# Optimization experiments

Measured on AMD Instinct MI355X. Metric: run time of the kernel, lower is better.

## Reference

```python
import jax, jax.numpy as jnp
import numpy as np

DIM = 512
HEADS = 8
HD = DIM // HEADS
WS = 4          # window_size
SHIFT = 2       # window_size // 2
HID = 4 * DIM   # mlp hidden
EPS = 1e-5


def _ln(x, g, b):
    m = jnp.mean(x, axis=-1, keepdims=True)
    v = jnp.mean((x - m) ** 2, axis=-1, keepdims=True)
    return (x - m) * jax.lax.rsqrt(v + EPS) * g + b


def setup_inputs() -> dict:
    key = jax.random.key(0)
    ks = jax.random.split(key, 12)
    s = 0.02
    return {
        "x": jax.random.normal(ks[0], (2, 32, 32, 32, DIM), dtype=jnp.float32),
        "ln1_g": jnp.ones((DIM,), jnp.float32),
        "ln1_b": jnp.zeros((DIM,), jnp.float32),
        "qkv_w": jax.random.normal(ks[1], (DIM, 3 * DIM), jnp.float32) * s,
        "qkv_b": jnp.zeros((3 * DIM,), jnp.float32),
        "proj_w": jax.random.normal(ks[2], (DIM, DIM), jnp.float32) * s,
        "proj_b": jnp.zeros((DIM,), jnp.float32),
        "ln2_g": jnp.ones((DIM,), jnp.float32),
        "ln2_b": jnp.zeros((DIM,), jnp.float32),
        "ffn_w1": jax.random.normal(ks[3], (DIM, HID), jnp.float32) * s,
        "ffn_b1": jnp.zeros((HID,), jnp.float32),
        "ffn_w2": jax.random.normal(ks[4], (HID, DIM), jnp.float32) * s,
        "ffn_b2": jnp.zeros((DIM,), jnp.float32),
    }


def reference(x, ln1_g, ln1_b, qkv_w, qkv_b, proj_w, proj_b,
              ln2_g, ln2_b, ffn_w1, ffn_b1, ffn_w2, ffn_b2):
    B, D, H, W, C = x.shape
    nD, nH, nW = D // WS, H // WS, W // WS
    N = WS ** 3

    # cyclic shift
    xs = jnp.roll(x, (-SHIFT, -SHIFT, -SHIFT), axis=(1, 2, 3))

    # window partition: (B*numWin, N, C)
    xw = xs.reshape(B, nD, WS, nH, WS, nW, WS, C)
    xw = xw.transpose(0, 1, 3, 5, 2, 4, 6, 7).reshape(-1, N, C)

    # pre-norm attention
    h = _ln(xw, ln1_g, ln1_b)
    qkv = (h @ qkv_w + qkv_b).reshape(-1, N, 3, HEADS, HD)
    q, k, v = jnp.moveaxis(qkv, 2, 0)          # each (Bn, N, HEADS, HD)
    scale = HD ** -0.5
    logits = jnp.einsum('bnhd,bmhd->bhnm', q, k) * scale
    attn = jax.nn.softmax(logits, axis=-1)
    out = jnp.einsum('bhnm,bmhd->bnhd', attn, v).reshape(-1, N, C)
    out = out @ proj_w + proj_b
    xw = xw + out

    # window reverse + unshift
    xo = xw.reshape(B, nD, nH, nW, WS, WS, WS, C)
    xo = xo.transpose(0, 1, 4, 2, 5, 3, 6, 7).reshape(B, D, H, W, C)
    xo = jnp.roll(xo, (SHIFT, SHIFT, SHIFT), axis=(1, 2, 3))

    # pre-norm FFN (exact GELU, dropout inactive in eval)
    h2 = _ln(xo, ln2_g, ln2_b)
    ffn = jax.nn.gelu(h2 @ ffn_w1 + ffn_b1, approximate=False) @ ffn_w2 + ffn_b2
    return xo + ffn
```

## Files before the change

### kernel.cpp

```cpp
#include <hip/hip_runtime.h>
#include <hip/hip_bf16.h>


typedef __attribute__((ext_vector_type(4))) short short4v;
typedef __attribute__((ext_vector_type(8))) short short8v;
typedef __attribute__((ext_vector_type(4))) float f32x4;

__device__ __forceinline__ unsigned short f2bf(float f) {
  unsigned u = __float_as_uint(f);
  u += 0x7fffu + ((u >> 16) & 1u);
  return (unsigned short)(u >> 16);
}

__device__ __forceinline__ void gload_lds16(const unsigned short* g, unsigned short* l) {
  __builtin_amdgcn_global_load_lds(
      (const __attribute__((address_space(1))) unsigned int*)g,
      (__attribute__((address_space(3))) unsigned int*)l, 16, 0, 0);
}

__global__ __launch_bounds__(256)
void wprep_all(const float* __restrict__ qkv_w, const float* __restrict__ proj_w,
               const float* __restrict__ w1, const float* __restrict__ w2,
               unsigned short* __restrict__ wt) {
  int idx = blockIdx.x * 256 + threadIdx.x;
  const float* w; int kbits, N, base;
  if (idx < 786432)       { w = qkv_w;  kbits = 9;  N = 1536; base = 0; }
  else if (idx < 1048576) { w = proj_w; kbits = 9;  N = 512;  base = 786432; }
  else if (idx < 2097152) { w = w1;     kbits = 9;  N = 2048; base = 1048576; }
  else                    { w = w2;     kbits = 11; N = 512;  base = 2097152; }
  int li = idx - base;
  int K = 1 << kbits;
  int n = li >> kbits, kk = li & (K - 1);
  wt[idx] = f2bf(w[(long)kk * N + n]);
}

__global__ __launch_bounds__(256)
void ln_kernel(const float* __restrict__ src, const float* __restrict__ g,
               const float* __restrict__ bb, unsigned short* __restrict__ dst,
               const int gather) {
  const int lane = threadIdx.x & 63;
  const int row = blockIdx.x * 4 + (threadIdx.x >> 6);
  long srow;
  if (gather) {
    int n = row & 63, win = row >> 6;
    int w0 = win & 7, h0 = (win >> 3) & 7, d0 = (win >> 6) & 7, b2 = win >> 9;
    int dx = n & 3, dy = (n >> 2) & 3, dz = n >> 4;
    int od = (d0 * 4 + dz + 2) & 31, oh = (h0 * 4 + dy + 2) & 31, ow = (w0 * 4 + dx + 2) & 31;
    srow = (((long)b2 * 32 + od) * 32 + oh) * 32 + ow;
  } else {
    srow = row;
  }
  const float4* sp = (const float4*)(src + srow * 512);
  float4 x0 = sp[lane], x1 = sp[lane + 64];
  float sum = x0.x + x0.y + x0.z + x0.w + x1.x + x1.y + x1.z + x1.w;
  float sq  = x0.x*x0.x + x0.y*x0.y + x0.z*x0.z + x0.w*x0.w
            + x1.x*x1.x + x1.y*x1.y + x1.z*x1.z + x1.w*x1.w;
#pragma unroll
  for (int off = 1; off < 64; off <<= 1) {
    sum += __shfl_xor(sum, off, 64);
    sq  += __shfl_xor(sq, off, 64);
  }
  float mean = sum * (1.0f / 512.0f);
  float var  = sq * (1.0f / 512.0f) - mean * mean;
  float rstd = rsqrtf(var + 1e-5f);
  float4 g0 = ((const float4*)g)[lane], g1 = ((const float4*)g)[lane + 64];
  float4 b0 = ((const float4*)bb)[lane], b1v = ((const float4*)bb)[lane + 64];
  ushort4 o0, o1;
  o0.x = f2bf((x0.x - mean) * rstd * g0.x + b0.x);
  o0.y = f2bf((x0.y - mean) * rstd * g0.y + b0.y);
  o0.z = f2bf((x0.z - mean) * rstd * g0.z + b0.z);
  o0.w = f2bf((x0.w - mean) * rstd * g0.w + b0.w);
  o1.x = f2bf((x1.x - mean) * rstd * g1.x + b1v.x);
  o1.y = f2bf((x1.y - mean) * rstd * g1.y + b1v.y);
  o1.z = f2bf((x1.z - mean) * rstd * g1.z + b1v.z);
  o1.w = f2bf((x1.w - mean) * rstd * g1.w + b1v.w);
  *(ushort4*)(dst + (long)row * 512 + lane * 4) = o0;
  *(ushort4*)(dst + (long)row * 512 + 256 + lane * 4) = o1;
}

template <int EPI>
__global__ __launch_bounds__(512, 2)
void gemm_bt(const unsigned short* __restrict__ A,
             const unsigned short* __restrict__ Bt,
             const float* __restrict__ bias, int K,
             void* __restrict__ out0,
             unsigned short* __restrict__ out1,
             unsigned short* __restrict__ out2,
             const float* __restrict__ res) {
  __shared__ unsigned short As[2][256 * 64];
  __shared__ unsigned short Bs[2][256 * 64];
  const int tid = threadIdx.x;
  const int lane = tid & 63;
  const int wv = tid >> 6;
  const int wm = wv >> 2;
  const int wn = wv & 3;
  const int quad = lane >> 4;
  const int l15 = lane & 15;

  const int gx = gridDim.x;
  const int nwg = gx * gridDim.y;
  const int bid = blockIdx.y * gx + blockIdx.x;
  const int cpx = nwg >> 3;
  const int wg2 = (bid & 7) * cpx + (bid >> 3);
  const int bx = wg2 % gx;
  const int by = wg2 / gx;
  const long row0 = (long)by * 256;
  const long col0 = (long)bx * 256;

  f32x4 acc[8][4] = {};

  const int srow = wv * 8 + (lane >> 3);
  const int scg  = (lane & 7) ^ (lane >> 3);
  const unsigned short* gA = A  + (row0 + srow) * K + scg * 8;
  const unsigned short* gB = Bt + (col0 + srow) * K + scg * 8;
  const long jmp = 64L * K;
  const int ldst = wv * 512;

#define STAGE_A(buf, koff) do {                                         \
    _Pragma("unroll")                                                   \
    for (int j = 0; j < 4; ++j)                                         \
      gload_lds16(gA + (koff) + j * jmp, &As[buf][ldst + j * 4096]);    \
  } while (0)
#define STAGE_B(buf, koff) do {                                         \
    _Pragma("unroll")                                                   \
    for (int j = 0; j < 4; ++j)                                         \
      gload_lds16(gB + (koff) + j * jmp, &Bs[buf][ldst + j * 4096]);    \
  } while (0)

  const int co0 = ((quad)     ^ (l15 & 7)) * 8;
  const int co1 = ((quad + 4) ^ (l15 & 7)) * 8;
  const int aB0 = (wm * 128 + l15) * 64 + co0;
  const int aB1 = (wm * 128 + l15) * 64 + co1;
  const int bB0 = (wn * 64 + l15) * 64 + co0;
  const int bB1 = (wn * 64 + l15) * 64 + co1;

#define MFMA_ROW(mh)                                                    \
    _Pragma("unroll")                                                   \
    for (int i = 0; i < 4; ++i)                                         \
      _Pragma("unroll")                                                 \
      for (int nt = 0; nt < 4; ++nt)                                    \
        acc[(mh) * 4 + i][nt] = __builtin_amdgcn_mfma_f32_16x16x32_bf16( \
            af[i], bfrag[nt], acc[(mh) * 4 + i][nt], 0, 0, 0)

  const int nk = K >> 6;
  STAGE_A(0, 0);
  STAGE_B(0, 0);
  asm volatile("s_waitcnt vmcnt(0)" ::: "memory");
  __builtin_amdgcn_s_barrier();

  for (int t = 0; t < nk; ++t) {
    const int cur = t & 1, nxt = cur ^ 1;
    const int more = (t + 1 < nk);
    const int kn = (t + 1) << 6;
    const unsigned short* Ac = As[cur];
    const unsigned short* Bc = Bs[cur];
    short8v bfrag[4];
    {
      short8v af[4];
#pragma unroll
      for (int nt = 0; nt < 4; ++nt) bfrag[nt] = *(const short8v*)&Bc[bB0 + nt * 1024];
#pragma unroll
      for (int i = 0; i < 4; ++i) af[i] = *(const short8v*)&Ac[aB0 + i * 1024];
      if (more) STAGE_A(nxt, kn);
      __builtin_amdgcn_s_barrier();
      __builtin_amdgcn_s_setprio(1);
      MFMA_ROW(0);
      __builtin_amdgcn_s_setprio(0);
      __builtin_amdgcn_s_barrier();
    }
    {
      short8v af[4];
#pragma unroll
      for (int i = 0; i < 4; ++i) af[i] = *(const short8v*)&Ac[aB0 + (4 + i) * 1024];
      if (more) STAGE_B(nxt, kn);
      __builtin_amdgcn_s_barrier();
      __builtin_amdgcn_s_setprio(1);
      MFMA_ROW(1);
      __builtin_amdgcn_s_setprio(0);
      __builtin_amdgcn_s_barrier();
    }
    {
      short8v af[4];
#pragma unroll
      for (int nt = 0; nt < 4; ++nt) bfrag[nt] = *(const short8v*)&Bc[bB1 + nt * 1024];
#pragma unroll
      for (int i = 0; i < 4; ++i) af[i] = *(const short8v*)&Ac[aB1 + i * 1024];
      __builtin_amdgcn_s_barrier();
      __builtin_amdgcn_s_setprio(1);
      MFMA_ROW(0);
      __builtin_amdgcn_s_setprio(0);
      __builtin_amdgcn_s_barrier();
    }
    {
      short8v af[4];
#pragma unroll
      for (int i = 0; i < 4; ++i) af[i] = *(const short8v*)&Ac[aB1 + (4 + i) * 1024];
      __builtin_amdgcn_s_barrier();
      __builtin_amdgcn_s_setprio(1);
      MFMA_ROW(1);
      __builtin_amdgcn_s_setprio(0);
      asm volatile("s_waitcnt vmcnt(0)" ::: "memory");
      __builtin_amdgcn_s_barrier();
    }
  }
#undef STAGE_A
#undef STAGE_B
#undef MFMA_ROW

#pragma unroll
  for (int mt = 0; mt < 8; ++mt) {
#pragma unroll
    for (int nt = 0; nt < 4; ++nt) {
#pragma unroll
      for (int r = 0; r < 4; ++r) {
        const long gr = row0 + wm * 128 + mt * 16 + quad * 4 + r;
        const long gc = col0 + wn * 64 + nt * 16 + l15;
        float val = acc[mt][nt][r] + bias[gc];
        if (EPI == 0) {
          int which = (int)(gc >> 9), rem = (int)gc & 511;
          int head = rem >> 6, hd = rem & 63;
          long win = gr >> 6, n = gr & 63;
          long base = (win * 8 + head) * 4096;
          unsigned short bv = f2bf(val);
          if (which == 0)      ((unsigned short*)out0)[base + n * 64 + hd] = bv;
          else if (which == 1) out1[base + n * 64 + hd] = bv;
          else                 out2[base + hd * 64 + n] = bv;
        } else if (EPI == 1) {
          int win = (int)(gr >> 6), n = (int)gr & 63;
          int w0 = win & 7, h0 = (win >> 3) & 7, d0 = (win >> 6) & 7, b2 = win >> 9;
          int dx = n & 3, dy = (n >> 2) & 3, dz = n >> 4;
          int od = (d0 * 4 + dz + 2) & 31, oh = (h0 * 4 + dy + 2) & 31, ow = (w0 * 4 + dx + 2) & 31;
          long addr = ((((long)b2 * 32 + od) * 32 + oh) * 32 + ow) * 512 + gc;
          ((float*)out0)[addr] = res[addr] + val;
        } else if (EPI == 2) {
          float ge = 0.5f * val * (1.0f + erff(val * 0.70710678118654752f));
          ((unsigned short*)out0)[gr * 2048 + gc] = f2bf(ge);
        } else {
          long addr = gr * 512 + gc;
          ((float*)out0)[addr] = res[addr] + val;
        }
      }
    }
  }
}

__global__ __launch_bounds__(256)
void attn_kernel(const unsigned short* __restrict__ q,
                 const unsigned short* __restrict__ k,
                 const unsigned short* __restrict__ vt,
                 unsigned short* __restrict__ out) {
  __shared__ unsigned short Ps[4][64 * 72];
  const int lane = threadIdx.x & 63;
  const int wave = threadIdx.x >> 6;
  const int quad = lane >> 4;
  const int l15 = lane & 15;
  const int unit = blockIdx.x * 4 + wave;
  const int win = unit >> 3;
  const int head = unit & 7;
  const long base = (long)unit * 4096;

  f32x4 s[4][4] = {};
#pragma unroll
  for (int kk = 0; kk < 64; kk += 32) {
    short8v a[4], b[4];
#pragma unroll
    for (int t = 0; t < 4; ++t) {
      a[t] = *(const short8v*)(q + base + (t * 16 + l15) * 64 + kk + quad * 8);
      b[t] = *(const short8v*)(k + base + (t * 16 + l15) * 64 + kk + quad * 8);
    }
#pragma unroll
    for (int mt = 0; mt < 4; ++mt)
#pragma unroll
      for (int nt = 0; nt < 4; ++nt)
        s[mt][nt] = __builtin_amdgcn_mfma_f32_16x16x32_bf16(a[mt], b[nt], s[mt][nt], 0, 0, 0);
  }

  float lrow[4][4];
#pragma unroll
  for (int mt = 0; mt < 4; ++mt) {
#pragma unroll
    for (int r = 0; r < 4; ++r) {
      float v0 = s[mt][0][r] * 0.125f, v1 = s[mt][1][r] * 0.125f;
      float v2 = s[mt][2][r] * 0.125f, v3 = s[mt][3][r] * 0.125f;
      float mx = fmaxf(fmaxf(v0, v1), fmaxf(v2, v3));
#pragma unroll
      for (int off = 1; off < 16; off <<= 1) mx = fmaxf(mx, __shfl_xor(mx, off, 64));
      v0 = __expf(v0 - mx); v1 = __expf(v1 - mx);
      v2 = __expf(v2 - mx); v3 = __expf(v3 - mx);
      float sm = v0 + v1 + v2 + v3;
#pragma unroll
      for (int off = 1; off < 16; off <<= 1) sm += __shfl_xor(sm, off, 64);
      lrow[mt][r] = sm;
      int row = mt * 16 + quad * 4 + r;
      Ps[wave][row * 72 + 0 + l15]  = f2bf(v0);
      Ps[wave][row * 72 + 16 + l15] = f2bf(v1);
      Ps[wave][row * 72 + 32 + l15] = f2bf(v2);
      Ps[wave][row * 72 + 48 + l15] = f2bf(v3);
    }
  }
  __syncthreads();

  f32x4 o[4][4] = {};
#pragma unroll
  for (int kk = 0; kk < 64; kk += 32) {
    short8v a[4], b[4];
#pragma unroll
    for (int t = 0; t < 4; ++t) {
      a[t] = *(const short8v*)(&Ps[wave][(t * 16 + l15) * 72 + kk + quad * 8]);
      b[t] = *(const short8v*)(vt + base + (t * 16 + l15) * 64 + kk + quad * 8);
    }
#pragma unroll
    for (int mt = 0; mt < 4; ++mt)
#pragma unroll
      for (int nt = 0; nt < 4; ++nt)
        o[mt][nt] = __builtin_amdgcn_mfma_f32_16x16x32_bf16(a[mt], b[nt], o[mt][nt], 0, 0, 0);
  }

#pragma unroll
  for (int mt = 0; mt < 4; ++mt)
#pragma unroll
    for (int nt = 0; nt < 4; ++nt)
#pragma unroll
      for (int r = 0; r < 4; ++r) {
        int row = mt * 16 + quad * 4 + r;
        int col = nt * 16 + l15;
        float val = o[mt][nt][r] / lrow[mt][r];
        out[((long)win * 64 + row) * 512 + head * 64 + col] = f2bf(val);
      }
}

extern "C" void kernel_launch(void* const* d_in, const int* in_sizes, int n_in,
                              void* d_out, int out_size, void* d_ws, size_t ws_size,
                              hipStream_t stream) {
  const float* x      = (const float*)d_in[0];
  const float* ln1_g  = (const float*)d_in[1];
  const float* ln1_b  = (const float*)d_in[2];
  const float* qkv_w  = (const float*)d_in[3];
  const float* qkv_b  = (const float*)d_in[4];
  const float* proj_w = (const float*)d_in[5];
  const float* proj_b = (const float*)d_in[6];
  const float* ln2_g  = (const float*)d_in[7];
  const float* ln2_b  = (const float*)d_in[8];
  const float* w1     = (const float*)d_in[9];
  const float* b1     = (const float*)d_in[10];
  const float* w2     = (const float*)d_in[11];
  const float* b2     = (const float*)d_in[12];

  char* ws = (char*)d_ws;
  unsigned short* wt_all  = (unsigned short*)ws;
  unsigned short* wt_qkv  = (unsigned short*)(ws + 0);
  unsigned short* wt_proj = (unsigned short*)(ws + 1572864);
  unsigned short* wt_1    = (unsigned short*)(ws + 2097152);
  unsigned short* wt_2    = (unsigned short*)(ws + 4194304);
  float*          xo      = (float*)(ws + 8388608);
  unsigned short* h       = (unsigned short*)(ws + 142606336);
  unsigned short* attno   = (unsigned short*)(ws + 209715200);
  unsigned short* qb      = (unsigned short*)(ws + 276824064);
  unsigned short* kb      = (unsigned short*)(ws + 343932928);
  unsigned short* vb      = (unsigned short*)(ws + 411041792);
  unsigned short* hid     = (unsigned short*)(ws + 209715200);
  float* out = (float*)d_out;

  wprep_all<<<12288, 256, 0, stream>>>(qkv_w, proj_w, w1, w2, wt_all);

  ln_kernel<<<16384, 256, 0, stream>>>(x, ln1_g, ln1_b, h, 1);
  gemm_bt<0><<<dim3(6, 256), 512, 0, stream>>>(h, wt_qkv, qkv_b, 512, qb, kb, vb, nullptr);
  attn_kernel<<<2048, 256, 0, stream>>>(qb, kb, vb, attno);
  gemm_bt<1><<<dim3(2, 256), 512, 0, stream>>>(attno, wt_proj, proj_b, 512, xo, nullptr, nullptr, x);
  ln_kernel<<<16384, 256, 0, stream>>>(xo, ln2_g, ln2_b, h, 0);
  gemm_bt<2><<<dim3(8, 256), 512, 0, stream>>>(h, wt_1, b1, 512, hid, nullptr, nullptr, nullptr);
  gemm_bt<3><<<dim3(2, 256), 512, 0, stream>>>(hid, wt_2, b2, 2048, out, nullptr, nullptr, xo);
}
```

Measured before the change: 1.107 ms.

## Simplify GEMM main loop to one barrier per k-step and use fast erf

Replaces the four-phase barrier-interleaved GEMM loop with a loop that prefetches both A and B tiles up front, loads all B fragments at once, and issues all MFMAs followed by one __syncthreads per k-step. It also swaps erff in the GELU epilogue for a polynomial erf approximation using hardware reciprocal and fast exp. The intent is to cut barrier overhead and transcendental cost. It trades away the fine-grained overlap of LDS reads with MFMA and raises register pressure.

```diff
diff --git a/kernel.cpp b/kernel.cpp
--- a/kernel.cpp
+++ b/kernel.cpp
@@ -10,6 +10,21 @@
   unsigned u = __float_as_uint(f);
   u += 0x7fffu + ((u >> 16) & 1u);
   return (unsigned short)(u >> 16);
+}
+
+__device__ __forceinline__ float erf_fast(float x) {
+  float ax = fabsf(x);
+  float y = 1.0f + 0.3275911f * ax;
+  float t;
+  asm("v_rcp_f32 %0, %1" : "=v"(t) : "v"(y));
+  float p = t * (0.254829592f +
+            t * (-0.284496736f +
+            t * (1.421413741f +
+            t * (-1.453152027f +
+            t * 1.061405429f))));
+  float e = __expf(-ax * ax);
+  float r = 1.0f - p * e;
+  return copysignf(r, x);
 }
 
 __device__ __forceinline__ void gload_lds16(const unsigned short* g, unsigned short* l) {
@@ -134,78 +149,53 @@
   const int bB0 = (wn * 64 + l15) * 64 + co0;
   const int bB1 = (wn * 64 + l15) * 64 + co1;
 
-#define MFMA_ROW(mh)                                                    \
-    _Pragma("unroll")                                                   \
-    for (int i = 0; i < 4; ++i)                                         \
-      _Pragma("unroll")                                                 \
-      for (int nt = 0; nt < 4; ++nt)                                    \
-        acc[(mh) * 4 + i][nt] = __builtin_amdgcn_mfma_f32_16x16x32_bf16( \
-            af[i], bfrag[nt], acc[(mh) * 4 + i][nt], 0, 0, 0)
-
   const int nk = K >> 6;
   STAGE_A(0, 0);
   STAGE_B(0, 0);
-  asm volatile("s_waitcnt vmcnt(0)" ::: "memory");
-  __builtin_amdgcn_s_barrier();
+  __syncthreads();
 
   for (int t = 0; t < nk; ++t) {
     const int cur = t & 1, nxt = cur ^ 1;
-    const int more = (t + 1 < nk);
-    const int kn = (t + 1) << 6;
     const unsigned short* Ac = As[cur];
     const unsigned short* Bc = Bs[cur];
-    short8v bfrag[4];
-    {
-      short8v af[4];
-#pragma unroll
-      for (int nt = 0; nt < 4; ++nt) bfrag[nt] = *(const short8v*)&Bc[bB0 + nt * 1024];
-#pragma unroll
-      for (int i = 0; i < 4; ++i) af[i] = *(const short8v*)&Ac[aB0 + i * 1024];
-      if (more) STAGE_A(nxt, kn);
-      __builtin_amdgcn_s_barrier();
+    if (t + 1 < nk) {
+      const int kn = (t + 1) << 6;
+      STAGE_A(nxt, kn);
+      STAGE_B(nxt, kn);
+    }
+    short8v bf0[4], bf1[4];
+#pragma unroll
+    for (int nt = 0; nt < 4; ++nt) {
+      bf0[nt] = *(const short8v*)&Bc[bB0 + nt * 1024];
+      bf1[nt] = *(const short8v*)&Bc[bB1 + nt * 1024];
+    }
+#pragma unroll
+    for (int mh = 0; mh < 2; ++mh) {
+      short8v af0[4], af1[4];
+#pragma unroll
+      for (int i = 0; i < 4; ++i) {
+        af0[i] = *(const short8v*)&Ac[aB0 + (mh * 4 + i) * 1024];
+        af1[i] = *(const short8v*)&Ac[aB1 + (mh * 4 + i) * 1024];
+      }
       __builtin_amdgcn_s_setprio(1);
-      MFMA_ROW(0);
+#pragma unroll
+      for (int i = 0; i < 4; ++i)
+#pragma unroll
+        for (int nt = 0; nt < 4; ++nt)
+          acc[mh * 4 + i][nt] = __builtin_amdgcn_mfma_f32_16x16x32_bf16(
+              af0[i], bf0[nt], acc[mh * 4 + i][nt], 0, 0, 0);
+#pragma unroll
+      for (int i = 0; i < 4; ++i)
+#pragma unroll
+        for (int nt = 0; nt < 4; ++nt)
+          acc[mh * 4 + i][nt] = __builtin_amdgcn_mfma_f32_16x16x32_bf16(
+              af1[i], bf1[nt], acc[mh * 4 + i][nt], 0, 0, 0);
       __builtin_amdgcn_s_setprio(0);
-      __builtin_amdgcn_s_barrier();
-    }
-    {
-      short8v af[4];
-#pragma unroll
-      for (int i = 0; i < 4; ++i) af[i] = *(const short8v*)&Ac[aB0 + (4 + i) * 1024];
-      if (more) STAGE_B(nxt, kn);
-      __builtin_amdgcn_s_barrier();
-      __builtin_amdgcn_s_setprio(1);
-      MFMA_ROW(1);
-      __builtin_amdgcn_s_setprio(0);
-      __builtin_amdgcn_s_barrier();
-    }
-    {
-      short8v af[4];
-#pragma unroll
-      for (int nt = 0; nt < 4; ++nt) bfrag[nt] = *(const short8v*)&Bc[bB1 + nt * 1024];
-#pragma unroll
-      for (int i = 0; i < 4; ++i) af[i] = *(const short8v*)&Ac[aB1 + i * 1024];
-      __builtin_amdgcn_s_barrier();
-      __builtin_amdgcn_s_setprio(1);
-      MFMA_ROW(0);
-      __builtin_amdgcn_s_setprio(0);
-      __builtin_amdgcn_s_barrier();
-    }
-    {
-      short8v af[4];
-#pragma unroll
-      for (int i = 0; i < 4; ++i) af[i] = *(const short8v*)&Ac[aB1 + (4 + i) * 1024];
-      __builtin_amdgcn_s_barrier();
-      __builtin_amdgcn_s_setprio(1);
-      MFMA_ROW(1);
-      __builtin_amdgcn_s_setprio(0);
-      asm volatile("s_waitcnt vmcnt(0)" ::: "memory");
-      __builtin_amdgcn_s_barrier();
-    }
+    }
+    __syncthreads();
   }
 #undef STAGE_A
 #undef STAGE_B
-#undef MFMA_ROW
 
 #pragma unroll
   for (int mt = 0; mt < 8; ++mt) {
@@ -233,7 +223,7 @@
           long addr = ((((long)b2 * 32 + od) * 32 + oh) * 32 + ow) * 512 + gc;
           ((float*)out0)[addr] = res[addr] + val;
         } else if (EPI == 2) {
-          float ge = 0.5f * val * (1.0f + erff(val * 0.70710678118654752f));
+          float ge = 0.5f * val * (1.0f + erf_fast(val * 0.70710678118654752f));
           ((unsigned short*)out0)[gr * 2048 + gc] = f2bf(ge);
         } else {
           long addr = gr * 512 + gc;
```

Measured after the change: 1.093 ms. About the same (-1.3%).
